# Performance work log

Measured on AMD Instinct MI355X. Metric: run time of the kernel, lower is better.

Reference implementation:

```python
import jax, jax.numpy as jnp
import numpy as np

N, E, G = 25600, 409600, 128   # nodes, edges, graphs
IN, H, C = 200, 4, 64          # raw feat dim, heads, hidden_channels
IN2 = 2 * IN                   # after NaN-mask concat
BN_EPS = 1e-5

def _glorot(key, shape):
    lim = float(np.sqrt(6.0 / (shape[0] + shape[-1])))
    return jax.random.uniform(key, shape, jnp.float32, -lim, lim)

def setup_inputs():
    key = jax.random.key(0)
    k = iter(jax.random.split(key, 40))
    inp = {
        "x": jax.random.normal(next(k), (N, IN), jnp.float32),
        "edge_index": jax.random.randint(next(k), (2, E), 0, N, jnp.int32),
        "edge_attr": jax.random.normal(next(k), (E, 1), jnp.float32),
        "batch": jnp.repeat(jnp.arange(G, dtype=jnp.int32), N // G),
    }
    dims = [(IN2, H, C), (H * C, H, C), (H * C, 1, C)]
    for i, (din, h, c) in enumerate(dims):
        inp[f"W{i}"] = _glorot(next(k), (din, h * c))
        inp[f"as{i}"] = _glorot(next(k), (h, c))
        inp[f"ad{i}"] = _glorot(next(k), (h, c))
        inp[f"We{i}"] = _glorot(next(k), (1, h * c))
        inp[f"ae{i}"] = _glorot(next(k), (h, c))
        inp[f"b{i}"] = jnp.zeros((h * c,), jnp.float32)
    inp["bn_g"] = jnp.ones((H * C,), jnp.float32)
    inp["bn_b"] = jnp.zeros((H * C,), jnp.float32)
    inp["bn_m"] = jnp.zeros((H * C,), jnp.float32)
    inp["bn_v"] = jnp.ones((H * C,), jnp.float32)
    inp["cw1"] = _glorot(next(k), (C, C))
    inp["cb1"] = jnp.zeros((C,), jnp.float32)
    inp["cw2"] = _glorot(next(k), (C, 2))
    inp["cb2"] = jnp.zeros((2,), jnp.float32)
    return inp

def _gat(x, src, dst, ea, W, att_s, att_d, We, att_e, b, heads, ch):
    """PyG GATConv (edge_dim=1, add_self_loops=True, fill_value='mean', concat=True)."""
    n = x.shape[0]
    # self-loop edge_attr = mean of incoming edge_attr per destination node
    cnt = jax.ops.segment_sum(jnp.ones((ea.shape[0], 1), ea.dtype), dst, n)
    loop_ea = jax.ops.segment_sum(ea, dst, n) / jnp.maximum(cnt, 1.0)
    idx = jnp.arange(n, dtype=src.dtype)
    src = jnp.concatenate([src, idx])
    dst = jnp.concatenate([dst, idx])
    ea = jnp.concatenate([ea, loop_ea], axis=0)
    h = (x @ W).reshape(n, heads, ch)                      # [N,H,C]
    a_s = jnp.einsum('nhc,hc->nh', h, att_s)
    a_d = jnp.einsum('nhc,hc->nh', h, att_d)
    a_e = jnp.einsum('ehc,hc->eh', (ea @ We).reshape(-1, heads, ch), att_e)
    alpha = jax.nn.leaky_relu(a_s[src] + a_d[dst] + a_e, 0.2)   # [E',H]
    # segment softmax over destination neighborhoods
    m = jax.ops.segment_max(alpha, dst, n)
    ex = jnp.exp(alpha - m[dst])
    z = jax.ops.segment_sum(ex, dst, n)
    alpha = ex / (z[dst] + 1e-16)
    out = jax.ops.segment_sum(h[src] * alpha[:, :, None], dst, n)  # [N,H,C]
    return out.reshape(n, heads * ch) + b

def reference(x, edge_index, edge_attr, batch,
              W0, as0, ad0, We0, ae0, b0,
              W1, as1, ad1, We1, ae1, b1,
              W2, as2, ad2, We2, ae2, b2,
              bn_g, bn_b, bn_m, bn_v, cw1, cb1, cw2, cb2):
    nan_mask = jnp.isnan(x).astype(x.dtype)
    x = jnp.concatenate([jnp.nan_to_num(x), nan_mask], axis=-1)   # [N, 2*IN]
    edge_attr = jnp.nan_to_num(edge_attr)
    src, dst = edge_index[0], edge_index[1]
    for (W, a_s, a_d, We, a_e, b) in [(W0, as0, ad0, We0, ae0, b0),
                                      (W1, as1, ad1, We1, ae1, b1)]:
        x = _gat(x, src, dst, edge_attr, W, a_s, a_d, We, a_e, b, H, C)
        x = (x - bn_m) / jnp.sqrt(bn_v + BN_EPS) * bn_g + bn_b    # eval-mode BN
        x = jax.nn.relu(x)                                        # dropout = identity (eval)
    x = _gat(x, src, dst, edge_attr, W2, as2, ad2, We2, ae2, b2, 1, C)
    # global mean pool over graphs
    cnt = jax.ops.segment_sum(jnp.ones((x.shape[0], 1), x.dtype), batch, G)
    g = jax.ops.segment_sum(x, batch, G) / jnp.maximum(cnt, 1.0)  # [G, C]
    hdn = jax.nn.gelu(g @ cw1 + cb1, approximate=False)
    return hdn @ cw2 + cb2                                        # [G, 2]
```

## Files before the change

kernel.cpp:

```cpp
#include <hip/hip_runtime.h>
#include <hip/hip_bf16.h>

static const int kN  = 25600;
static const int kE  = 409600;
static const int kG  = 128;
static const int kNPG = 200;
static const int kIN = 200;
static const int kIN2 = 400;
static const int kK0 = 448;
static const int kMD = 64;
#define BN_EPS_ 1e-5f

typedef __attribute__((ext_vector_type(8))) short short8;
typedef __attribute__((ext_vector_type(4))) ushort us4;
typedef __attribute__((ext_vector_type(4))) float f32x4;

__device__ __forceinline__ float bu(ushort u) {
  union { float f; unsigned u32; } x; x.u32 = ((unsigned)u) << 16; return x.f;
}
__device__ __forceinline__ ushort f2u(float v) {
  __hip_bfloat16 t = __float2bfloat16(v);
  return *(ushort*)&t;
}
__device__ __forceinline__ float wredSum(float v) {
#pragma unroll
  for (int off = 1; off < 64; off <<= 1) v += __shfl_xor(v, off, 64);
  return v;
}
__device__ __forceinline__ float lrelu(float a) { return (a > 0.f) ? a : 0.2f * a; }

#define GLOAD16(g, l) __builtin_amdgcn_global_load_lds( \
    (const __attribute__((address_space(1))) unsigned int*)(g), \
    (__attribute__((address_space(3))) unsigned int*)(l), 16, 0, 0)

__global__ void k_pre(const float* __restrict__ x, ushort* __restrict__ x2,
                      const float* __restrict__ W0, ushort* __restrict__ Wt0,
                      const float* __restrict__ W1, ushort* __restrict__ Wt1,
                      const float* __restrict__ W2, ushort* __restrict__ Wt2,
                      const float* __restrict__ We0, const float* __restrict__ ae0,
                      const float* __restrict__ We1, const float* __restrict__ ae1,
                      const float* __restrict__ We2, const float* __restrict__ ae2,
                      float* __restrict__ wed,
                      const int* __restrict__ ei, const float* __restrict__ ea,
                      int2* __restrict__ epk, int* __restrict__ deg) {
  int b = blockIdx.x, tid = threadIdx.x;
  if (b < 5000) {
    int i4 = (b * 256 + tid) * 4;
    int n = i4 / kIN, j = i4 - n * kIN;
    float4 v = *(const float4*)&x[i4];
    ushort o0[4], o1[4];
    float vv[4] = {v.x, v.y, v.z, v.w};
#pragma unroll
    for (int q = 0; q < 4; q++) {
      bool bad = (vv[q] != vv[q]);
      o0[q] = f2u(bad ? 0.f : vv[q]);
      o1[q] = f2u(bad ? 1.f : 0.f);
    }
    *(us4*)&x2[(size_t)n * kK0 + j] = *(us4*)o0;
    *(us4*)&x2[(size_t)n * kK0 + kIN + j] = *(us4*)o1;
    return;
  }
  int pb = b - 5000;
  if (pb >= 2323) {
    int idx = (pb - 2323) * 256 + tid;
    short8 z = {0, 0, 0, 0, 0, 0, 0, 0};
    if (idx < 153600) {
      int row = idx / 6, c = idx - row * 6;
      *(short8*)&x2[(size_t)row * kK0 + kIN2 + c * 8] = z;
    } else {
      int j = idx - 153600;
      if (j < 1536) {
        int row = j / 6, c = j - row * 6;
        *(short8*)&Wt0[(size_t)row * kK0 + kIN2 + c * 8] = z;
      }
    }
    return;
  }
  if (pb >= 723) {
    int e = (pb - 723) * 256 + tid;
    int d = ei[kE + e];
    int s = ei[e];
    float v = ea[e];
    if (v != v) v = 0.f;
    int slot = atomicAdd(&deg[d], 1);
    if (slot < kMD) {
      int2 rec; rec.x = s; rec.y = __float_as_int(v);
      epk[(size_t)d * kMD + slot] = rec;
    }
    return;
  }
  if (pb >= 720) {
    int l = pb - 720;
    const float* We = (l == 0) ? We0 : (l == 1) ? We1 : We2;
    const float* ae = (l == 0) ? ae0 : (l == 1) ? ae1 : ae2;
    int n = (l == 2) ? 64 : 256;
    float v = (tid < n) ? We[tid] * ae[tid] : 0.f;
    v = wredSum(v);
    if ((tid & 63) == 0 && tid < n) wed[l * 4 + (tid >> 6)] = v;
    return;
  }
  int i = pb * 256 + tid;
  if (i < 102400) {
    int n = i / kIN2, k = i - n * kIN2;
    Wt0[(size_t)n * kK0 + k] = f2u(W0[(size_t)k * 256 + n]);
  } else if (i < 102400 + 65536) {
    int j = i - 102400;
    int n = j >> 8, k = j & 255;
    Wt1[(size_t)n * 256 + k] = f2u(W1[(size_t)k * 256 + n]);
  } else {
    int j = i - 102400 - 65536;
    int n = j >> 8, k = j & 255;
    Wt2[(size_t)n * 256 + k] = f2u(W2[(size_t)k * 64 + n]);
  }
}

template <int BN, int MT, bool AHM>
__global__ __launch_bounds__(256) void k_gemm_f(const ushort* __restrict__ A,
                                                const ushort* __restrict__ Bt,
                                                ushort* __restrict__ C,
                                                const float* __restrict__ as_g,
                                                const float* __restrict__ ad_g,
                                                float* __restrict__ a_sg,
                                                float* __restrict__ a_dg, int K) {
  constexpr int MI = (BN == 256) ? (MT / 16) : 1;
  __shared__ ushort As[MT * 64];
  __shared__ ushort Bs[BN * 64];
  int tid = threadIdx.x;
  int lane = tid & 63, w = tid >> 6;
  int l15 = lane & 15, l4 = lane >> 4;
  int row0 = blockIdx.y * MT;
  int wr = (BN == 256) ? 0 : (w * 16);
  int wc = (BN == 256) ? (w * 64) : 0;
  f32x4 acc[MI][4] = {};
  int srow = lane >> 3;
  int schunk = lane & 7;

  for (int kt = 0; kt < K; kt += 64) {
    __syncthreads();
#pragma unroll
    for (int i = 0; i < MT / 32; i++) {
      int ra = w * (MT / 4) + i * 8;
      int r = ra + srow;
      const ushort* ap = AHM
          ? &A[(size_t)(kt >> 6) * ((size_t)kN * 64) + (size_t)(row0 + r) * 64 +
               ((schunk ^ (r & 7)) * 8)]
          : &A[(size_t)(row0 + r) * K + kt + ((schunk ^ (r & 7)) * 8)];
      GLOAD16(ap, &As[ra * 64]);
    }
#pragma unroll
    for (int i = 0; i < BN / 32; i++) {
      int rb = w * (BN / 4) + i * 8;
      int r = rb + srow;
      GLOAD16(&Bt[(size_t)r * K + kt + ((schunk ^ (r & 7)) * 8)],
              &Bs[rb * 64]);
    }
    __syncthreads();
#pragma unroll
    for (int kk = 0; kk < 2; kk++) {
      short8 af[MI], bf[4];
#pragma unroll
      for (int mi = 0; mi < MI; mi++) {
        int r = wr + mi * 16 + l15;
        af[mi] = *(const short8*)&As[r * 64 + ((kk * 32 + l4 * 8) ^ ((r & 7) * 8))];
      }
#pragma unroll
      for (int ni = 0; ni < 4; ni++) {
        int r = wc + ni * 16 + l15;
        bf[ni] = *(const short8*)&Bs[r * 64 + ((kk * 32 + l4 * 8) ^ ((r & 7) * 8))];
      }
#pragma unroll
      for (int mi = 0; mi < MI; mi++)
#pragma unroll
        for (int ni = 0; ni < 4; ni++)
          acc[mi][ni] = __builtin_amdgcn_mfma_f32_16x16x32_bf16(af[mi], bf[ni],
                                                                acc[mi][ni], 0, 0, 0);
    }
  }
#pragma unroll
  for (int mi = 0; mi < MI; mi++) {
    int rbase = row0 + wr + mi * 16 + l4 * 4;
#pragma unroll
    for (int ni = 0; ni < 4; ni++) {
      int col = wc + ni * 16 + l15;
#pragma unroll
      for (int r = 0; r < 4; r++) {
        size_t caddr = (BN == 256)
            ? ((size_t)w * ((size_t)kN * 64) + (size_t)(rbase + r) * 64 + (col & 63))
            : ((size_t)(rbase + r) * BN + col);
        C[caddr] = f2u(acc[mi][ni][r]);
      }
    }
  }
  float asv[4], adv[4];
#pragma unroll
  for (int ni = 0; ni < 4; ni++) {
    asv[ni] = as_g[wc + ni * 16 + l15];
    adv[ni] = ad_g[wc + ni * 16 + l15];
  }
#pragma unroll
  for (int mi = 0; mi < MI; mi++) {
#pragma unroll
    for (int r = 0; r < 4; r++) {
      float ps = 0.f, pd = 0.f;
#pragma unroll
      for (int ni = 0; ni < 4; ni++) {
        ps += acc[mi][ni][r] * asv[ni];
        pd += acc[mi][ni][r] * adv[ni];
      }
#pragma unroll
      for (int off = 1; off < 16; off <<= 1) {
        ps += __shfl_xor(ps, off, 64);
        pd += __shfl_xor(pd, off, 64);
      }
      if (l15 == 0) {
        int row = row0 + wr + mi * 16 + l4 * 4 + r;
        size_t aaddr = (BN == 256) ? ((size_t)w * kN + row) : (size_t)row;
        a_sg[aaddr] = ps;
        a_dg[aaddr] = pd;
      }
    }
  }
}

__global__ __launch_bounds__(256) void k_agg4(
    const ushort* __restrict__ hbuf, const int2* __restrict__ epk,
    const int* __restrict__ deg, const float* __restrict__ a_s,
    const float* __restrict__ a_d, const float* __restrict__ wed,
    const float* __restrict__ bias, const float* __restrict__ bng,
    const float* __restrict__ bnb, const float* __restrict__ bnm,
    const float* __restrict__ bnv, ushort* __restrict__ xout) {
  __shared__ float lds_w[4][kMD];
  __shared__ int   lds_s[4][kMD];
  int tid = threadIdx.x;
  int w = tid >> 6, lane = tid & 63;
  int bid = blockIdx.x;
  int r8 = bid & 7;
  int head = r8 >> 1;
  int dgroup = (r8 & 1) * 3200 + (bid >> 3);
  int d = dgroup * 4 + w;
  const ushort* hb = hbuf + (size_t)head * kN * 64;
  const float* asg = a_s + (size_t)head * kN;
  const int2* rp = &epk[(size_t)d * kMD];
  int dgt = deg[d];
  int dg = min(dgt, kMD);
  float adh = a_d[(size_t)head * kN + d];
  float wdh = wed[head];

  float wv = 0.f, ev = 0.f;
  if (lane < dg) {
    int2 rec = rp[lane];
    ev = __int_as_float(rec.y);
    wv = __expf(lrelu(asg[rec.x] + adh + ev * wdh));
    lds_w[w][lane] = wv;
    lds_s[w][lane] = rec.x;
  }
  float szp = wv, seap = ev;
#pragma unroll
  for (int off = 1; off < 64; off <<= 1) {
    szp  += __shfl_xor(szp, off, 64);
    seap += __shfl_xor(seap, off, 64);
  }
  float lea = seap / fmaxf((float)dgt, 1.f);
  float selfw = __expf(lrelu(asg[d] + adh + lea * wdh));
  float winv = 1.f / (szp + selfw + 1e-16f);

  int e4 = lane >> 4;
  int c4 = (lane & 15) * 4;
  float a0 = 0.f, a1 = 0.f, a2 = 0.f, a3 = 0.f;
  int k = 0;
  for (; k + 16 <= dg; k += 16) {
    int s4[4]; float w4[4];
#pragma unroll
    for (int j = 0; j < 4; j++) {
      s4[j] = lds_s[w][k + j * 4 + e4];
      w4[j] = lds_w[w][k + j * 4 + e4];
    }
    ushort4 v4[4];
#pragma unroll
    for (int j = 0; j < 4; j++)
      v4[j] = *(const ushort4*)&hb[(size_t)s4[j] * 64 + c4];
#pragma unroll
    for (int j = 0; j < 4; j++) {
      a0 += w4[j] * bu(v4[j].x); a1 += w4[j] * bu(v4[j].y);
      a2 += w4[j] * bu(v4[j].z); a3 += w4[j] * bu(v4[j].w);
    }
  }
  for (; k + 4 <= dg; k += 4) {
    int s0 = lds_s[w][k + e4];
    float w0 = lds_w[w][k + e4];
    ushort4 v0 = *(const ushort4*)&hb[(size_t)s0 * 64 + c4];
    a0 += w0 * bu(v0.x); a1 += w0 * bu(v0.y);
    a2 += w0 * bu(v0.z); a3 += w0 * bu(v0.w);
  }
  if (k + e4 < dg) {
    int s0 = lds_s[w][k + e4];
    float w0 = lds_w[w][k + e4];
    ushort4 v0 = *(const ushort4*)&hb[(size_t)s0 * 64 + c4];
    a0 += w0 * bu(v0.x); a1 += w0 * bu(v0.y);
    a2 += w0 * bu(v0.z); a3 += w0 * bu(v0.w);
  }
  a0 += __shfl_xor(a0, 16, 64); a0 += __shfl_xor(a0, 32, 64);
  a1 += __shfl_xor(a1, 16, 64); a1 += __shfl_xor(a1, 32, 64);
  a2 += __shfl_xor(a2, 16, 64); a2 += __shfl_xor(a2, 32, 64);
  a3 += __shfl_xor(a3, 16, 64); a3 += __shfl_xor(a3, 32, 64);

  if (e4 == 0) {
    ushort4 vs = *(const ushort4*)&hb[(size_t)d * 64 + c4];
    a0 += selfw * bu(vs.x); a1 += selfw * bu(vs.y);
    a2 += selfw * bu(vs.z); a3 += selfw * bu(vs.w);
    int c = head * 64 + c4;
    float4 bi = *(const float4*)&bias[c];
    a0 = a0 * winv + bi.x; a1 = a1 * winv + bi.y;
    a2 = a2 * winv + bi.z; a3 = a3 * winv + bi.w;
    float4 g4 = *(const float4*)&bng[c], b4 = *(const float4*)&bnb[c];
    float4 m4 = *(const float4*)&bnm[c], v4 = *(const float4*)&bnv[c];
    a0 = fmaxf((a0 - m4.x) * rsqrtf(v4.x + BN_EPS_) * g4.x + b4.x, 0.f);
    a1 = fmaxf((a1 - m4.y) * rsqrtf(v4.y + BN_EPS_) * g4.y + b4.y, 0.f);
    a2 = fmaxf((a2 - m4.z) * rsqrtf(v4.z + BN_EPS_) * g4.z + b4.z, 0.f);
    a3 = fmaxf((a3 - m4.w) * rsqrtf(v4.w + BN_EPS_) * g4.w + b4.w, 0.f);
    ushort4 o = make_ushort4(f2u(a0), f2u(a1), f2u(a2), f2u(a3));
    *(ushort4*)&xout[(size_t)head * kN * 64 + (size_t)d * 64 + c4] = o;
  }
}

__global__ __launch_bounds__(256) void k_agg1(
    const ushort* __restrict__ hbuf, const int2* __restrict__ epk,
    const int* __restrict__ deg, const float* __restrict__ a_s,
    const float* __restrict__ a_d, const float* __restrict__ wed,
    float* __restrict__ gsum) {
  __shared__ float lds_w[4][kMD];
  __shared__ int   lds_s[4][kMD];
  __shared__ float part[4][64];
  int tid = threadIdx.x;
  int w = tid >> 6, lane = tid & 63;
  int d = blockIdx.x * 4 + w;
  const int2* rp = &epk[(size_t)d * kMD];
  int dgt = deg[d];
  int dg = min(dgt, kMD);
  float adh = a_d[d];
  float wdh = wed[0];

  float wv = 0.f, ev = 0.f;
  if (lane < dg) {
    int2 rec = rp[lane];
    ev = __int_as_float(rec.y);
    wv = __expf(lrelu(a_s[rec.x] + adh + ev * wdh));
    lds_w[w][lane] = wv;
    lds_s[w][lane] = rec.x;
  }
  float szp = wv, seap = ev;
#pragma unroll
  for (int off = 1; off < 64; off <<= 1) {
    szp  += __shfl_xor(szp, off, 64);
    seap += __shfl_xor(seap, off, 64);
  }
  float lea = seap / fmaxf((float)dgt, 1.f);
  float selfw = __expf(lrelu(a_s[d] + adh + lea * wdh));
  float winv = 1.f / (szp + selfw + 1e-16f);

  float vselff = bu(hbuf[(size_t)d * 64 + lane]);
  float acc = 0.f;
  int k = 0;
  for (; k + 16 <= dg; k += 16) {
    int s16[16]; float w16[16];
#pragma unroll
    for (int j = 0; j < 16; j++) {
      s16[j] = lds_s[w][k + j];
      w16[j] = lds_w[w][k + j];
    }
    ushort v16[16];
#pragma unroll
    for (int j = 0; j < 16; j++) v16[j] = hbuf[(size_t)s16[j] * 64 + lane];
#pragma unroll
    for (int j = 0; j < 16; j++) acc += w16[j] * bu(v16[j]);
  }
  for (; k + 8 <= dg; k += 8) {
    int s8[8]; float w8[8];
#pragma unroll
    for (int j = 0; j < 8; j++) {
      s8[j] = lds_s[w][k + j];
      w8[j] = lds_w[w][k + j];
    }
    ushort v8[8];
#pragma unroll
    for (int j = 0; j < 8; j++) v8[j] = hbuf[(size_t)s8[j] * 64 + lane];
#pragma unroll
    for (int j = 0; j < 8; j++) acc += w8[j] * bu(v8[j]);
  }
  for (; k < dg; k++) {
    acc += lds_w[w][k] * bu(hbuf[(size_t)lds_s[w][k] * 64 + lane]);
  }
  acc += selfw * vselff;
  acc = acc * winv;

  part[w][lane] = acc;
  __syncthreads();
  if (w == 0) {
    float s = (part[0][lane] + part[1][lane]) + (part[2][lane] + part[3][lane]);
    int g = (blockIdx.x * 4) / kNPG;
    atomicAdd(&gsum[g * 64 + lane], s);
  }
}

__global__ void k_head(const float* __restrict__ gsum, const float* __restrict__ bias,
                       const float* __restrict__ cw1, const float* __restrict__ cb1,
                       const float* __restrict__ cw2, const float* __restrict__ cb2,
                       float* __restrict__ out) {
  __shared__ float gb[64], hb[64];
  int g = blockIdx.x, c = threadIdx.x;
  gb[c] = gsum[g * 64 + c] * (1.f / kNPG) + bias[c];
  __syncthreads();
  float s = cb1[c];
#pragma unroll 8
  for (int i = 0; i < 64; i++) s += gb[i] * cw1[i * 64 + c];
  s = 0.5f * s * (1.f + erff(s * 0.70710678118654752f));
  hb[c] = s;
  __syncthreads();
  if (c < 2) {
    float o = cb2[c];
    for (int i = 0; i < 64; i++) o += hb[i] * cw2[i * 2 + c];
    out[g * 2 + c] = o;
  }
}


extern "C" void kernel_launch(void* const* d_in, const int* in_sizes, int n_in,
                              void* d_out, int out_size, void* d_ws, size_t ws_size,
                              hipStream_t stream) {
  (void)in_sizes; (void)n_in; (void)out_size; (void)ws_size;
  const float* x  = (const float*)d_in[0];
  const int* ei   = (const int*)d_in[1];
  const float* ea = (const float*)d_in[2];
  const float *W[3], *as_[3], *ad_[3], *We[3], *ae[3], *bi[3];
  for (int l = 0; l < 3; l++) {
    W[l]   = (const float*)d_in[4 + l * 6 + 0];
    as_[l] = (const float*)d_in[4 + l * 6 + 1];
    ad_[l] = (const float*)d_in[4 + l * 6 + 2];
    We[l]  = (const float*)d_in[4 + l * 6 + 3];
    ae[l]  = (const float*)d_in[4 + l * 6 + 4];
    bi[l]  = (const float*)d_in[4 + l * 6 + 5];
  }
  const float* bng = (const float*)d_in[22];
  const float* bnb = (const float*)d_in[23];
  const float* bnm = (const float*)d_in[24];
  const float* bnv = (const float*)d_in[25];
  const float* cw1 = (const float*)d_in[26];
  const float* cb1 = (const float*)d_in[27];
  const float* cw2 = (const float*)d_in[28];
  const float* cb2 = (const float*)d_in[29];

  char* p = (char*)d_ws;
  auto alloc = [&](size_t bytes) -> void* {
    void* r = (void*)p;
    p += (bytes + 255) & ~(size_t)255;
    return r;
  };
  ushort* x2b   = (ushort*)alloc((size_t)kN * kK0 * 2);
  ushort* hbufb = (ushort*)alloc((size_t)kN * 256 * 2);
  ushort* xbA   = (ushort*)alloc((size_t)kN * 256 * 2);
  ushort* xbB   = (ushort*)alloc((size_t)kN * 256 * 2);
  ushort* Wt0   = (ushort*)alloc((size_t)kK0 * 256 * 2);
  ushort* Wt1   = (ushort*)alloc((size_t)256 * 256 * 2);
  ushort* Wt2   = (ushort*)alloc((size_t)256 * 64 * 2);
  float* a_s    = (float*)alloc((size_t)kN * 4 * 4);
  float* a_d    = (float*)alloc((size_t)kN * 4 * 4);
  int2* epk     = (int2*)alloc((size_t)kN * kMD * 8);
  float* wed    = (float*)alloc(256);
  int* deg      = (int*)alloc((size_t)kN * 4);
  float* gsum   = (float*)alloc((size_t)kG * 64 * 4);

  hipMemsetAsync(deg, 0, (size_t)kN * 4 + (size_t)kG * 64 * 4, stream);
  k_pre<<<5000 + 2929, 256, 0, stream>>>(
      x, x2b, W[0], Wt0, W[1], Wt1, W[2], Wt2, We[0], ae[0], We[1], ae[1],
      We[2], ae[2], wed, ei, ea, epk, deg);
  dim3 gg64m(1, kN / 64);
  k_gemm_f<256, 64, false><<<gg64m, 256, 0, stream>>>(
      x2b, Wt0, hbufb, as_[0], ad_[0], a_s, a_d, kK0);
  k_agg4<<<kN, 256, 0, stream>>>(hbufb, epk, deg, a_s, a_d,
                                 &wed[0], bi[0], bng, bnb, bnm, bnv, xbA);
  k_gemm_f<256, 64, true><<<gg64m, 256, 0, stream>>>(
      xbA, Wt1, hbufb, as_[1], ad_[1], a_s, a_d, 256);
  k_agg4<<<kN, 256, 0, stream>>>(hbufb, epk, deg, a_s, a_d,
                                 &wed[4], bi[1], bng, bnb, bnm, bnv, xbB);
  dim3 gg64(1, kN / 64);
  k_gemm_f<64, 64, true><<<gg64, 256, 0, stream>>>(
      xbB, Wt2, hbufb, as_[2], ad_[2], a_s, a_d, 256);
  k_agg1<<<kN / 4, 256, 0, stream>>>(hbufb, epk, deg, a_s, a_d, &wed[8], gsum);
  k_head<<<kG, 64, 0, stream>>>(gsum, bi[2], cw1, cb1, cw2, cb2, (float*)d_out);
}
```

Measured before the change: 320.1 us.

## Process 16 destination nodes per block in multi-head GAT aggregation

Restructures the per-head aggregation kernel so each block handles 16 destination nodes instead of 4. Edge-weight computation is spread over 16 lanes per node, with the normalizer and self-loop weight staged in shared memory, followed by a block barrier. Each wave then aggregates four nodes in sequence. This cuts the block count by four and is meant to raise the useful work per wave in the weight phase, since average degree is around 16. In exchange it adds a __syncthreads, serializes gathers across nodes within a wave, and uses more LDS per block.

```diff
diff --git a/kernel.cpp b/kernel.cpp
--- a/kernel.cpp
+++ b/kernel.cpp
@@ -229,97 +229,115 @@
     const float* __restrict__ bias, const float* __restrict__ bng,
     const float* __restrict__ bnb, const float* __restrict__ bnm,
     const float* __restrict__ bnv, ushort* __restrict__ xout) {
-  __shared__ float lds_w[4][kMD];
-  __shared__ int   lds_s[4][kMD];
+  __shared__ float lds_w[16][kMD];
+  __shared__ int   lds_s[16][kMD];
+  __shared__ float lds_m[16][2];
   int tid = threadIdx.x;
-  int w = tid >> 6, lane = tid & 63;
   int bid = blockIdx.x;
   int r8 = bid & 7;
   int head = r8 >> 1;
-  int dgroup = (r8 & 1) * 3200 + (bid >> 3);
-  int d = dgroup * 4 + w;
+  int dgroup = (r8 & 1) * 800 + (bid >> 3);
+  int dbase = dgroup * 16;
   const ushort* hb = hbuf + (size_t)head * kN * 64;
   const float* asg = a_s + (size_t)head * kN;
-  const int2* rp = &epk[(size_t)d * kMD];
-  int dgt = deg[d];
-  int dg = min(dgt, kMD);
-  float adh = a_d[(size_t)head * kN + d];
   float wdh = wed[head];
 
-  float wv = 0.f, ev = 0.f;
-  if (lane < dg) {
-    int2 rec = rp[lane];
-    ev = __int_as_float(rec.y);
-    wv = __expf(lrelu(asg[rec.x] + adh + ev * wdh));
-    lds_w[w][lane] = wv;
-    lds_s[w][lane] = rec.x;
-  }
-  float szp = wv, seap = ev;
-#pragma unroll
-  for (int off = 1; off < 64; off <<= 1) {
-    szp  += __shfl_xor(szp, off, 64);
-    seap += __shfl_xor(seap, off, 64);
-  }
-  float lea = seap / fmaxf((float)dgt, 1.f);
-  float selfw = __expf(lrelu(asg[d] + adh + lea * wdh));
-  float winv = 1.f / (szp + selfw + 1e-16f);
-
+  {
+    int di = tid >> 4, slot0 = tid & 15;
+    int d = dbase + di;
+    int dgt = deg[d];
+    int dg = min(dgt, kMD);
+    float adh = a_d[(size_t)head * kN + d];
+    const int2* rp = &epk[(size_t)d * kMD];
+    float szp = 0.f, seap = 0.f;
+    for (int t = slot0; t < dg; t += 16) {
+      int2 rec = rp[t];
+      float ev = __int_as_float(rec.y);
+      float wv = __expf(lrelu(asg[rec.x] + adh + ev * wdh));
+      lds_w[di][t] = wv;
+      lds_s[di][t] = rec.x;
+      szp += wv;
+      seap += ev;
+    }
+#pragma unroll
+    for (int off = 1; off < 16; off <<= 1) {
+      szp  += __shfl_xor(szp, off, 64);
+      seap += __shfl_xor(seap, off, 64);
+    }
+    if (slot0 == 0) {
+      float lea = seap / fmaxf((float)dgt, 1.f);
+      float selfw = __expf(lrelu(asg[d] + adh + lea * wdh));
+      lds_m[di][0] = 1.f / (szp + selfw + 1e-16f);
+      lds_m[di][1] = selfw;
+    }
+  }
+  __syncthreads();
+
+  int w = tid >> 6, lane = tid & 63;
   int e4 = lane >> 4;
   int c4 = (lane & 15) * 4;
-  float a0 = 0.f, a1 = 0.f, a2 = 0.f, a3 = 0.f;
-  int k = 0;
-  for (; k + 16 <= dg; k += 16) {
-    int s4[4]; float w4[4];
-#pragma unroll
-    for (int j = 0; j < 4; j++) {
-      s4[j] = lds_s[w][k + j * 4 + e4];
-      w4[j] = lds_w[w][k + j * 4 + e4];
-    }
-    ushort4 v4[4];
-#pragma unroll
-    for (int j = 0; j < 4; j++)
-      v4[j] = *(const ushort4*)&hb[(size_t)s4[j] * 64 + c4];
-#pragma unroll
-    for (int j = 0; j < 4; j++) {
-      a0 += w4[j] * bu(v4[j].x); a1 += w4[j] * bu(v4[j].y);
-      a2 += w4[j] * bu(v4[j].z); a3 += w4[j] * bu(v4[j].w);
-    }
-  }
-  for (; k + 4 <= dg; k += 4) {
-    int s0 = lds_s[w][k + e4];
-    float w0 = lds_w[w][k + e4];
-    ushort4 v0 = *(const ushort4*)&hb[(size_t)s0 * 64 + c4];
-    a0 += w0 * bu(v0.x); a1 += w0 * bu(v0.y);
-    a2 += w0 * bu(v0.z); a3 += w0 * bu(v0.w);
-  }
-  if (k + e4 < dg) {
-    int s0 = lds_s[w][k + e4];
-    float w0 = lds_w[w][k + e4];
-    ushort4 v0 = *(const ushort4*)&hb[(size_t)s0 * 64 + c4];
-    a0 += w0 * bu(v0.x); a1 += w0 * bu(v0.y);
-    a2 += w0 * bu(v0.z); a3 += w0 * bu(v0.w);
-  }
-  a0 += __shfl_xor(a0, 16, 64); a0 += __shfl_xor(a0, 32, 64);
-  a1 += __shfl_xor(a1, 16, 64); a1 += __shfl_xor(a1, 32, 64);
-  a2 += __shfl_xor(a2, 16, 64); a2 += __shfl_xor(a2, 32, 64);
-  a3 += __shfl_xor(a3, 16, 64); a3 += __shfl_xor(a3, 32, 64);
-
-  if (e4 == 0) {
-    ushort4 vs = *(const ushort4*)&hb[(size_t)d * 64 + c4];
-    a0 += selfw * bu(vs.x); a1 += selfw * bu(vs.y);
-    a2 += selfw * bu(vs.z); a3 += selfw * bu(vs.w);
-    int c = head * 64 + c4;
-    float4 bi = *(const float4*)&bias[c];
-    a0 = a0 * winv + bi.x; a1 = a1 * winv + bi.y;
-    a2 = a2 * winv + bi.z; a3 = a3 * winv + bi.w;
-    float4 g4 = *(const float4*)&bng[c], b4 = *(const float4*)&bnb[c];
-    float4 m4 = *(const float4*)&bnm[c], v4 = *(const float4*)&bnv[c];
-    a0 = fmaxf((a0 - m4.x) * rsqrtf(v4.x + BN_EPS_) * g4.x + b4.x, 0.f);
-    a1 = fmaxf((a1 - m4.y) * rsqrtf(v4.y + BN_EPS_) * g4.y + b4.y, 0.f);
-    a2 = fmaxf((a2 - m4.z) * rsqrtf(v4.z + BN_EPS_) * g4.z + b4.z, 0.f);
-    a3 = fmaxf((a3 - m4.w) * rsqrtf(v4.w + BN_EPS_) * g4.w + b4.w, 0.f);
-    ushort4 o = make_ushort4(f2u(a0), f2u(a1), f2u(a2), f2u(a3));
-    *(ushort4*)&xout[(size_t)head * kN * 64 + (size_t)d * 64 + c4] = o;
+#pragma unroll
+  for (int j = 0; j < 4; j++) {
+    int di = w * 4 + j;
+    int d = dbase + di;
+    int dg = min(deg[d], kMD);
+    float a0 = 0.f, a1 = 0.f, a2 = 0.f, a3 = 0.f;
+    int k = 0;
+    for (; k + 16 <= dg; k += 16) {
+      int s4[4]; float w4[4];
+#pragma unroll
+      for (int q = 0; q < 4; q++) {
+        s4[q] = lds_s[di][k + q * 4 + e4];
+        w4[q] = lds_w[di][k + q * 4 + e4];
+      }
+      ushort4 v4[4];
+#pragma unroll
+      for (int q = 0; q < 4; q++)
+        v4[q] = *(const ushort4*)&hb[(size_t)s4[q] * 64 + c4];
+#pragma unroll
+      for (int q = 0; q < 4; q++) {
+        a0 += w4[q] * bu(v4[q].x); a1 += w4[q] * bu(v4[q].y);
+        a2 += w4[q] * bu(v4[q].z); a3 += w4[q] * bu(v4[q].w);
+      }
+    }
+    for (; k + 4 <= dg; k += 4) {
+      int s0 = lds_s[di][k + e4];
+      float w0 = lds_w[di][k + e4];
+      ushort4 v0 = *(const ushort4*)&hb[(size_t)s0 * 64 + c4];
+      a0 += w0 * bu(v0.x); a1 += w0 * bu(v0.y);
+      a2 += w0 * bu(v0.z); a3 += w0 * bu(v0.w);
+    }
+    if (k + e4 < dg) {
+      int s0 = lds_s[di][k + e4];
+      float w0 = lds_w[di][k + e4];
+      ushort4 v0 = *(const ushort4*)&hb[(size_t)s0 * 64 + c4];
+      a0 += w0 * bu(v0.x); a1 += w0 * bu(v0.y);
+      a2 += w0 * bu(v0.z); a3 += w0 * bu(v0.w);
+    }
+    a0 += __shfl_xor(a0, 16, 64); a0 += __shfl_xor(a0, 32, 64);
+    a1 += __shfl_xor(a1, 16, 64); a1 += __shfl_xor(a1, 32, 64);
+    a2 += __shfl_xor(a2, 16, 64); a2 += __shfl_xor(a2, 32, 64);
+    a3 += __shfl_xor(a3, 16, 64); a3 += __shfl_xor(a3, 32, 64);
+
+    if (e4 == 0) {
+      float winv = lds_m[di][0];
+      float sw   = lds_m[di][1];
+      ushort4 vs = *(const ushort4*)&hb[(size_t)d * 64 + c4];
+      a0 += sw * bu(vs.x); a1 += sw * bu(vs.y);
+      a2 += sw * bu(vs.z); a3 += sw * bu(vs.w);
+      int c = head * 64 + c4;
+      float4 bi = *(const float4*)&bias[c];
+      a0 = a0 * winv + bi.x; a1 = a1 * winv + bi.y;
+      a2 = a2 * winv + bi.z; a3 = a3 * winv + bi.w;
+      float4 g4 = *(const float4*)&bng[c], b4 = *(const float4*)&bnb[c];
+      float4 m4 = *(const float4*)&bnm[c], v4 = *(const float4*)&bnv[c];
+      a0 = fmaxf((a0 - m4.x) * rsqrtf(v4.x + BN_EPS_) * g4.x + b4.x, 0.f);
+      a1 = fmaxf((a1 - m4.y) * rsqrtf(v4.y + BN_EPS_) * g4.y + b4.y, 0.f);
+      a2 = fmaxf((a2 - m4.z) * rsqrtf(v4.z + BN_EPS_) * g4.z + b4.z, 0.f);
+      a3 = fmaxf((a3 - m4.w) * rsqrtf(v4.w + BN_EPS_) * g4.w + b4.w, 0.f);
+      ushort4 o = make_ushort4(f2u(a0), f2u(a1), f2u(a2), f2u(a3));
+      *(ushort4*)&xout[(size_t)head * kN * 64 + (size_t)d * 64 + c4] = o;
+    }
   }
 }
 
@@ -476,12 +494,12 @@
   dim3 gg64m(1, kN / 64);
   k_gemm_f<256, 64, false><<<gg64m, 256, 0, stream>>>(
       x2b, Wt0, hbufb, as_[0], ad_[0], a_s, a_d, kK0);
-  k_agg4<<<kN, 256, 0, stream>>>(hbufb, epk, deg, a_s, a_d,
-                                 &wed[0], bi[0], bng, bnb, bnm, bnv, xbA);
+  k_agg4<<<6400, 256, 0, stream>>>(hbufb, epk, deg, a_s, a_d,
+                                   &wed[0], bi[0], bng, bnb, bnm, bnv, xbA);
   k_gemm_f<256, 64, true><<<gg64m, 256, 0, stream>>>(
       xbA, Wt1, hbufb, as_[1], ad_[1], a_s, a_d, 256);
-  k_agg4<<<kN, 256, 0, stream>>>(hbufb, epk, deg, a_s, a_d,
-                                 &wed[4], bi[1], bng, bnb, bnm, bnv, xbB);
+  k_agg4<<<6400, 256, 0, stream>>>(hbufb, epk, deg, a_s, a_d,
+                                   &wed[4], bi[1], bng, bnb, bnm, bnv, xbB);
   dim3 gg64(1, kN / 64);
   k_gemm_f<64, 64, true><<<gg64, 256, 0, stream>>>(
       xbB, Wt2, hbufb, as_[2], ad_[2], a_s, a_d, 256);
```

After: 319.6 us. No clear change (-0.1%).
